# Optimization experiments

Measured on AMD Instinct MI355X. Metric: run time of the kernel, lower is better.

The kernel has to match this reference:

```python
import jax, jax.numpy as jnp
import numpy as np

B, N, D = 8192, 49, 3
D3 = 42  # embed_dim // 3
E = 128
K = 3    # min(3, N-1) nearest neighbors for local density


def setup_inputs() -> dict:
    key = jax.random.key(0)
    ks = jax.random.split(key, 8)
    points = jax.random.normal(ks[0], (B, N, D), jnp.float32)
    return {
        "points": points,
        "W_dist": jax.random.normal(ks[1], (1, D3), jnp.float32) * 1.0,
        "b_dist": jnp.zeros((D3,), jnp.float32),
        "emb": jax.random.normal(ks[2], (50, D3), jnp.float32) * 0.02,
        "W_den": jax.random.normal(ks[3], (1, D3), jnp.float32) * 1.0,
        "b_den": jnp.zeros((D3,), jnp.float32),
        "W_out": jax.random.normal(ks[4], (3 * D3, E), jnp.float32) * (1.0 / np.sqrt(3 * D3)),
        "b_out": jnp.zeros((E,), jnp.float32),
    }


def _local_density(points):
    # Batched cdist with diagonal masked to +inf, then mean of K smallest dists.
    sq = jnp.sum(points * points, axis=-1)                      # [B,N]
    d2 = sq[:, :, None] + sq[:, None, :] \
         - 2.0 * jnp.einsum('bnd,bmd->bnm', points, points)      # [B,N,N]
    d2 = jnp.maximum(d2, 0.0)
    eye = jnp.eye(points.shape[1], dtype=bool)
    d2 = jnp.where(eye, jnp.inf, d2)
    dists = jnp.sqrt(d2)
    nearest = -jax.lax.top_k(-dists, K)[0]                      # [B,N,K] smallest
    return jnp.mean(nearest, axis=-1, keepdims=True)            # [B,N,1]


def reference(points, W_dist, b_dist, emb, W_den, b_den, W_out, b_out):
    b, n, _ = points.shape
    centroid = jnp.mean(points, axis=1, keepdims=True)          # [B,1,3]
    rel = points - centroid
    centroid_dist = jnp.linalg.norm(rel, axis=-1, keepdims=True)  # [B,N,1]
    dist_f = centroid_dist @ W_dist + b_dist                    # [B,N,D3]
    # n_valid == N (no mask), a constant index into the count embedding
    count_f = jnp.broadcast_to(emb[n][None, None, :], (b, n, emb.shape[1]))
    density = _local_density(points)                            # [B,N,1]
    den_f = density @ W_den + b_den                             # [B,N,D3]
    features = jnp.concatenate([dist_f, count_f, den_f], axis=-1)  # [B,N,3*D3]
    return features @ W_out + b_out                             # [B,N,E]
```

## Files before the change

### kernel.cpp

```cpp
#include <hip/hip_runtime.h>
#include <math.h>

#define N_   49
#define D3_  42
#define E_   128
#define WAVES_PER_BLOCK 4

__global__ void precompute_uvc(const float* __restrict__ W_dist,
                               const float* __restrict__ b_dist,
                               const float* __restrict__ emb,
                               const float* __restrict__ W_den,
                               const float* __restrict__ b_den,
                               const float* __restrict__ W_out,
                               const float* __restrict__ b_out,
                               float* __restrict__ uvc) {
    int e = threadIdx.x;
    if (e >= E_) return;
    const float* embN = emb + N_ * D3_;
    float u = 0.f, v = 0.f, c = b_out[e];
    for (int j = 0; j < D3_; ++j) {
        float w0 = W_out[j * E_ + e];
        float w1 = W_out[(D3_ + j) * E_ + e];
        float w2 = W_out[(2 * D3_ + j) * E_ + e];
        u = fmaf(W_dist[j], w0, u);
        v = fmaf(W_den[j], w2, v);
        c = fmaf(b_dist[j], w0, c);
        c = fmaf(embN[j], w1, c);
        c = fmaf(b_den[j], w2, c);
    }
    uvc[e]          = u;
    uvc[E_ + e]     = v;
    uvc[2 * E_ + e] = c;
}

__global__ __launch_bounds__(256) void fused_rank2(
        const float* __restrict__ points,
        const float4* __restrict__ uvc4,
        float4* __restrict__ out4,
        int B) {
    __shared__ float  pts[WAVES_PER_BLOCK][N_ * 3];
    __shared__ float2 cdden[WAVES_PER_BLOCK][N_];

    const int lane = threadIdx.x & 63;
    const int w    = threadIdx.x >> 6;
    const long long b = (long long)blockIdx.x * WAVES_PER_BLOCK + w;
    if (b >= B) return;

    const int q = lane & 31;
    const float4 u = uvc4[q];
    const float4 v = uvc4[32 + q];
    const float4 c = uvc4[64 + q];

    const float* pb = points + b * (N_ * 3);
    for (int i = lane; i < N_ * 3; i += 64) pts[w][i] = pb[i];

    if (lane < N_) {
        const float px = pts[w][3 * lane], py = pts[w][3 * lane + 1],
                    pz = pts[w][3 * lane + 2];
        float sx = 0.f, sy = 0.f, sz = 0.f;
        float s0 = INFINITY, s1 = INFINITY, s2 = INFINITY;
        for (int m = 0; m < N_; ++m) {
            float qx = pts[w][3 * m], qy = pts[w][3 * m + 1], qz = pts[w][3 * m + 2];
            sx += qx; sy += qy; sz += qz;
            float dx = px - qx, dy = py - qy, dz = pz - qz;
            float d2 = fmaf(dx, dx, fmaf(dy, dy, dz * dz));
            if (m != lane) {
                if (d2 < s0)      { s2 = s1; s1 = s0; s0 = d2; }
                else if (d2 < s1) { s2 = s1; s1 = d2; }
                else if (d2 < s2) { s2 = d2; }
            }
        }
        const float inv = 1.0f / (float)N_;
        float cx = sx * inv, cy = sy * inv, cz = sz * inv;
        float dx = px - cx, dy = py - cy, dz = pz - cz;
        float cd  = sqrtf(fmaf(dx, dx, fmaf(dy, dy, dz * dz)));
        float den = (sqrtf(s0) + sqrtf(s1) + sqrtf(s2)) * (1.0f / 3.0f);
        cdden[w][lane] = make_float2(cd, den);
    }

    float4* ob = out4 + b * (long long)(N_ * 32);
    #pragma unroll 5
    for (int j = 0; j < 25; ++j) {
        int g = j * 64 + lane;
        if (g < N_ * 32) {
            int row = g >> 5;
            float2 ad = cdden[w][row];
            float4 r;
            r.x = fmaf(ad.x, u.x, fmaf(ad.y, v.x, c.x));
            r.y = fmaf(ad.x, u.y, fmaf(ad.y, v.y, c.y));
            r.z = fmaf(ad.x, u.z, fmaf(ad.y, v.z, c.z));
            r.w = fmaf(ad.x, u.w, fmaf(ad.y, v.w, c.w));
            ob[g] = r;
        }
    }
}

extern "C" void kernel_launch(void* const* d_in, const int* in_sizes, int n_in,
                              void* d_out, int out_size, void* d_ws, size_t ws_size,
                              hipStream_t stream) {
    const float* points = (const float*)d_in[0];
    const float* W_dist = (const float*)d_in[1];
    const float* b_dist = (const float*)d_in[2];
    const float* emb    = (const float*)d_in[3];
    const float* W_den  = (const float*)d_in[4];
    const float* b_den  = (const float*)d_in[5];
    const float* W_out  = (const float*)d_in[6];
    const float* b_out  = (const float*)d_in[7];

    float* uvc = (float*)d_ws;

    const int B = in_sizes[0] / (N_ * 3);
    const int nblocks = (B + WAVES_PER_BLOCK - 1) / WAVES_PER_BLOCK;

    precompute_uvc<<<1, 128, 0, stream>>>(W_dist, b_dist, emb, W_den, b_den,
                                          W_out, b_out, uvc);
    fused_rank2<<<nblocks, 64 * WAVES_PER_BLOCK, 0, stream>>>(
        points, (const float4*)uvc, (float4*)d_out, B);
}
```

Measured before the change: 228.5 us.

## Fuse weight folding into main kernel and process two batches per wave with prefetch

Merges the u/v/c precompute kernel into the main kernel: each block recomputes the folded weights into shared memory, so the second launch and the global round trip go away. Each wave now handles two batch elements, with the second element's points prefetched into registers while the first is being processed. Per-point results are broadcast with wave shuffles instead of going through shared memory. The cost is redundant weight folding in every block (42-step loops reading W_out) plus a block barrier, and the grid shrinks by half.

```diff
diff --git a/kernel.cpp b/kernel.cpp
--- a/kernel.cpp
+++ b/kernel.cpp
@@ -1,97 +1,136 @@
 #include <hip/hip_runtime.h>
 #include <math.h>
 
-#define N_   49
-#define D3_  42
-#define E_   128
-#define WAVES_PER_BLOCK 4
+#define N_     49
+#define D3_    42
+#define E_     128
+#define WPB    4
+#define ROUNDS 2
 
-__global__ void precompute_uvc(const float* __restrict__ W_dist,
-                               const float* __restrict__ b_dist,
-                               const float* __restrict__ emb,
-                               const float* __restrict__ W_den,
-                               const float* __restrict__ b_den,
-                               const float* __restrict__ W_out,
-                               const float* __restrict__ b_out,
-                               float* __restrict__ uvc) {
-    int e = threadIdx.x;
-    if (e >= E_) return;
-    const float* embN = emb + N_ * D3_;
-    float u = 0.f, v = 0.f, c = b_out[e];
-    for (int j = 0; j < D3_; ++j) {
-        float w0 = W_out[j * E_ + e];
-        float w1 = W_out[(D3_ + j) * E_ + e];
-        float w2 = W_out[(2 * D3_ + j) * E_ + e];
-        u = fmaf(W_dist[j], w0, u);
-        v = fmaf(W_den[j], w2, v);
-        c = fmaf(b_dist[j], w0, c);
-        c = fmaf(embN[j], w1, c);
-        c = fmaf(b_den[j], w2, c);
-    }
-    uvc[e]          = u;
-    uvc[E_ + e]     = v;
-    uvc[2 * E_ + e] = c;
-}
 
-__global__ __launch_bounds__(256) void fused_rank2(
+#define KNN(W, CD, DN) do {                                                  \
+    const int n = (lane < N_) ? lane : N_ - 1;                               \
+    const float px = pts[W][3*n], py = pts[W][3*n+1], pz = pts[W][3*n+2];    \
+    float sx = 0.f, sy = 0.f, sz = 0.f;                                      \
+    float t0 = INFINITY, t1 = INFINITY, t2 = INFINITY;                       \
+    for (int m = 0; m < N_; ++m) {                                           \
+        float qx = pts[W][3*m], qy = pts[W][3*m+1], qz = pts[W][3*m+2];      \
+        sx += qx; sy += qy; sz += qz;                                        \
+        float dx = px - qx, dy = py - qy, dz = pz - qz;                      \
+        float d2 = fmaf(dx, dx, fmaf(dy, dy, dz * dz));                      \
+        if (m != n) {                                                        \
+            if (d2 < t0)      { t2 = t1; t1 = t0; t0 = d2; }                 \
+            else if (d2 < t1) { t2 = t1; t1 = d2; }                          \
+            else if (d2 < t2) { t2 = d2; }                                   \
+        }                                                                    \
+    }                                                                        \
+    const float inv = 1.0f / (float)N_;                                      \
+    float cx = sx*inv, cy = sy*inv, cz = sz*inv;                             \
+    float ex = px-cx, ey = py-cy, ez = pz-cz;                                \
+    CD = sqrtf(fmaf(ex, ex, fmaf(ey, ey, ez * ez)));                         \
+    DN = (sqrtf(t0) + sqrtf(t1) + sqrtf(t2)) * (1.0f / 3.0f);                \
+} while (0)
+
+#define STORES(BB, CD, DN) do {                                              \
+    float4* ob = out4 + (long long)(BB) * (N_ * 32);                         \
+    _Pragma("unroll")                                                        \
+    for (int j = 0; j < 25; ++j) {                                           \
+        int row = 2*j + (lane >> 5);                                         \
+        float a = __shfl(CD, row);                                           \
+        float d = __shfl(DN, row);                                           \
+        if (row < N_) {                                                      \
+            float4 r;                                                        \
+            r.x = fmaf(a, u4.x, fmaf(d, v4.x, c4.x));                        \
+            r.y = fmaf(a, u4.y, fmaf(d, v4.y, c4.y));                        \
+            r.z = fmaf(a, u4.z, fmaf(d, v4.z, c4.z));                        \
+            r.w = fmaf(a, u4.w, fmaf(d, v4.w, c4.w));                        \
+            ob[row * 32 + q] = r;                                            \
+        }                                                                    \
+    }                                                                        \
+} while (0)
+
+__global__ __launch_bounds__(256) void fused_all(
         const float* __restrict__ points,
-        const float4* __restrict__ uvc4,
+        const float* __restrict__ W_dist,
+        const float* __restrict__ b_dist,
+        const float* __restrict__ emb,
+        const float* __restrict__ W_den,
+        const float* __restrict__ b_den,
+        const float* __restrict__ W_out,
+        const float* __restrict__ b_out,
         float4* __restrict__ out4,
         int B) {
-    __shared__ float  pts[WAVES_PER_BLOCK][N_ * 3];
-    __shared__ float2 cdden[WAVES_PER_BLOCK][N_];
+    __shared__ float pts[WPB][N_ * 3];
+    __shared__ __align__(16) float sUVC[3 * E_];
 
-    const int lane = threadIdx.x & 63;
-    const int w    = threadIdx.x >> 6;
-    const long long b = (long long)blockIdx.x * WAVES_PER_BLOCK + w;
-    if (b >= B) return;
+    const int tid    = threadIdx.x;
+    const int lane   = tid & 63;
+    const int w      = tid >> 6;
+    const int nwaves = gridDim.x * WPB;
+    const int wid    = blockIdx.x * WPB + w;
 
-    const int q = lane & 31;
-    const float4 u = uvc4[q];
-    const float4 v = uvc4[32 + q];
-    const float4 c = uvc4[64 + q];
-
-    const float* pb = points + b * (N_ * 3);
-    for (int i = lane; i < N_ * 3; i += 64) pts[w][i] = pb[i];
-
-    if (lane < N_) {
-        const float px = pts[w][3 * lane], py = pts[w][3 * lane + 1],
-                    pz = pts[w][3 * lane + 2];
-        float sx = 0.f, sy = 0.f, sz = 0.f;
-        float s0 = INFINITY, s1 = INFINITY, s2 = INFINITY;
-        for (int m = 0; m < N_; ++m) {
-            float qx = pts[w][3 * m], qy = pts[w][3 * m + 1], qz = pts[w][3 * m + 2];
-            sx += qx; sy += qy; sz += qz;
-            float dx = px - qx, dy = py - qy, dz = pz - qz;
-            float d2 = fmaf(dx, dx, fmaf(dy, dy, dz * dz));
-            if (m != lane) {
-                if (d2 < s0)      { s2 = s1; s1 = s0; s0 = d2; }
-                else if (d2 < s1) { s2 = s1; s1 = d2; }
-                else if (d2 < s2) { s2 = d2; }
-            }
-        }
-        const float inv = 1.0f / (float)N_;
-        float cx = sx * inv, cy = sy * inv, cz = sz * inv;
-        float dx = px - cx, dy = py - cy, dz = pz - cz;
-        float cd  = sqrtf(fmaf(dx, dx, fmaf(dy, dy, dz * dz)));
-        float den = (sqrtf(s0) + sqrtf(s1) + sqrtf(s2)) * (1.0f / 3.0f);
-        cdden[w][lane] = make_float2(cd, den);
+    const long long b0 = wid;
+    const bool v0 = (b0 < B);
+    float s0a = 0.f, s0b = 0.f, s0c = 0.f;
+    if (v0) {
+        const float* pb = points + b0 * (N_ * 3);
+        s0a = pb[lane];
+        s0b = pb[64 + lane];
+        if (lane < N_ * 3 - 128) s0c = pb[128 + lane];
     }
 
-    float4* ob = out4 + b * (long long)(N_ * 32);
-    #pragma unroll 5
-    for (int j = 0; j < 25; ++j) {
-        int g = j * 64 + lane;
-        if (g < N_ * 32) {
-            int row = g >> 5;
-            float2 ad = cdden[w][row];
-            float4 r;
-            r.x = fmaf(ad.x, u.x, fmaf(ad.y, v.x, c.x));
-            r.y = fmaf(ad.x, u.y, fmaf(ad.y, v.y, c.y));
-            r.z = fmaf(ad.x, u.z, fmaf(ad.y, v.z, c.z));
-            r.w = fmaf(ad.x, u.w, fmaf(ad.y, v.w, c.w));
-            ob[g] = r;
+    if (tid < E_) {
+        const float* embN = emb + N_ * D3_;
+        float u = 0.f, vv = 0.f, c = b_out[tid];
+        for (int j = 0; j < D3_; ++j) {
+            float w0 = W_out[j * E_ + tid];
+            float w1 = W_out[(D3_ + j) * E_ + tid];
+            float w2 = W_out[(2 * D3_ + j) * E_ + tid];
+            u  = fmaf(W_dist[j], w0, u);
+            vv = fmaf(W_den[j],  w2, vv);
+            c  = fmaf(b_dist[j], w0, c);
+            c  = fmaf(embN[j],   w1, c);
+            c  = fmaf(b_den[j],  w2, c);
         }
+        sUVC[tid]          = u;
+        sUVC[E_ + tid]     = vv;
+        sUVC[2 * E_ + tid] = c;
+    }
+
+    if (v0) {
+        pts[w][lane]      = s0a;
+        pts[w][64 + lane] = s0b;
+        if (lane < N_ * 3 - 128) pts[w][128 + lane] = s0c;
+    }
+
+    const long long b1 = (long long)wid + nwaves;
+    const bool v1 = (b1 < B);
+    float s1a = 0.f, s1b = 0.f, s1c = 0.f;
+    if (v1) {
+        const float* pb = points + b1 * (N_ * 3);
+        s1a = pb[lane];
+        s1b = pb[64 + lane];
+        if (lane < N_ * 3 - 128) s1c = pb[128 + lane];
+    }
+
+    float cd0 = 0.f, dn0 = 0.f;
+    if (v0) { KNN(w, cd0, dn0); }
+
+    __syncthreads();
+    const int q = lane & 31;
+    const float4 u4 = *(const float4*)&sUVC[4 * q];
+    const float4 v4 = *(const float4*)&sUVC[E_ + 4 * q];
+    const float4 c4 = *(const float4*)&sUVC[2 * E_ + 4 * q];
+
+    if (v0) { STORES(b0, cd0, dn0); }
+
+    if (v1) {
+        pts[w][lane]      = s1a;
+        pts[w][64 + lane] = s1b;
+        if (lane < N_ * 3 - 128) pts[w][128 + lane] = s1c;
+        float cd1, dn1;
+        KNN(w, cd1, dn1);
+        STORES(b1, cd1, dn1);
     }
 }
 
@@ -107,13 +146,10 @@
     const float* W_out  = (const float*)d_in[6];
     const float* b_out  = (const float*)d_in[7];
 
-    float* uvc = (float*)d_ws;
+    const int B = in_sizes[0] / (N_ * 3);
+    const int nblocks = (B + WPB * ROUNDS - 1) / (WPB * ROUNDS);
 
-    const int B = in_sizes[0] / (N_ * 3);
-    const int nblocks = (B + WAVES_PER_BLOCK - 1) / WAVES_PER_BLOCK;
-
-    precompute_uvc<<<1, 128, 0, stream>>>(W_dist, b_dist, emb, W_den, b_den,
-                                          W_out, b_out, uvc);
-    fused_rank2<<<nblocks, 64 * WAVES_PER_BLOCK, 0, stream>>>(
-        points, (const float4*)uvc, (float4*)d_out, B);
+    fused_all<<<nblocks, 64 * WPB, 0, stream>>>(
+        points, W_dist, b_dist, emb, W_den, b_den, W_out, b_out,
+        (float4*)d_out, B);
 }
```

Measured after the change: 225.8 us. Within noise of the previous version (-1.2%).
